# Performance work log

Measured on AMD Instinct MI355X. Metric: run time of the kernel, lower is better.

## Reference

```python
import jax, jax.numpy as jnp
import numpy as np

NUM_NODES = 8192
IN_FEATURES = 1024
OUT_FEATURES = 512
NUM_EDGES = 262144  # avg degree 32


def setup_inputs() -> dict:
    key = jax.random.key(0)
    k_x, k_w, k_b, k_src, k_dst = jax.random.split(key, 5)
    x = jax.random.normal(k_x, (NUM_NODES, IN_FEATURES), dtype=jnp.float32)
    # torch nn.Linear layout: weight [out, in], bias [out]
    W = jax.random.normal(k_w, (OUT_FEATURES, IN_FEATURES), dtype=jnp.float32) * (1.0 / np.sqrt(IN_FEATURES))
    b = jax.random.normal(k_b, (OUT_FEATURES,), dtype=jnp.float32) * 0.01
    src = jax.random.randint(k_src, (NUM_EDGES,), 0, NUM_NODES, dtype=jnp.int64)
    dst = jax.random.randint(k_dst, (NUM_EDGES,), 0, NUM_NODES, dtype=jnp.int64)
    edge_index = jnp.stack([src, dst], axis=0)
    return {"x": x, "W": W, "b": b, "edge_index": edge_index, "num_nodes": NUM_NODES}


def reference(x, W, b, edge_index, num_nodes):
    # Faithful to the torch module: build dense adjacency from edge list
    # (duplicate edges collapse to 1.0 via assignment semantics),
    # linear, (dropout p=0 -> identity), dense adj @ hidden, relu.
    adj = jnp.zeros((num_nodes, num_nodes), dtype=x.dtype)
    adj = adj.at[edge_index[0], edge_index[1]].set(1.0)
    hidden = x @ W.T + b            # [N, out]
    support = adj @ hidden          # [N, out] aggregation over neighbors
    return jax.nn.relu(support)
```

## Files before the change

kernel.cpp:

```cpp
#include <hip/hip_runtime.h>

#define N_NODES 8192
#define IN_F    1024
#define OUT_F   512
#define N_EDGES 262144
#define STRIDE  96
#define NBLK    64
#define EPB     (N_EDGES / NBLK)

#define HID_OFF     0u
#define WB_OFF      8388608u
#define DEG_OFF     9437184u
#define COL_OFF     9469952u
#define BH_OFF      12615680u
#define BO_OFF      14712832u
#define MAX_DEG     STRIDE

typedef short  bf16x8 __attribute__((ext_vector_type(8)));
typedef float  f32x4  __attribute__((ext_vector_type(4)));

__device__ __forceinline__ unsigned f2bf(float f) {
    unsigned u = __float_as_uint(f);
    u += 0x7fffu + ((u >> 16) & 1u);
    return u >> 16;
}

__device__ __forceinline__ float bflo(unsigned u) { return __uint_as_float(u << 16); }
__device__ __forceinline__ float bfhi(unsigned u) { return __uint_as_float(u & 0xffff0000u); }

__device__ __forceinline__ void ld_lds16(const void* g, void* l) {
    __builtin_amdgcn_global_load_lds(
        (const __attribute__((address_space(1))) void*)g,
        (__attribute__((address_space(3))) void*)l, 16, 0, 0);
}

#define NW8 (OUT_F * IN_F / 8)
__global__ __launch_bounds__(256) void prep_hist(const float* __restrict__ w,
                                                 unsigned short* __restrict__ wb,
                                                 const int* __restrict__ src,
                                                 int* __restrict__ blkhist) {
    __shared__ int h[N_NODES];
    const int bid = blockIdx.x;
    const int tid = threadIdx.x;

    if (bid < 256) {
        int i = bid * 256 + tid;
        const f32x4* p = (const f32x4*)w + (size_t)i * 2;
        f32x4 v0 = __builtin_nontemporal_load(p);
        f32x4 v1 = __builtin_nontemporal_load(p + 1);
        uint4 o;
        o.x = f2bf(v0.x) | (f2bf(v0.y) << 16);
        o.y = f2bf(v0.z) | (f2bf(v0.w) << 16);
        o.z = f2bf(v1.x) | (f2bf(v1.y) << 16);
        o.w = f2bf(v1.z) | (f2bf(v1.w) << 16);
        *((uint4*)wb + i) = o;
        return;
    }
    const int b = bid - 256;
    for (int i = tid; i < N_NODES; i += 256) h[i] = 0;
    __syncthreads();
    const int e0 = b * EPB;
#pragma unroll
    for (int j = 0; j < EPB / 256; ++j)
        atomicAdd(&h[src[e0 + j * 256 + tid]], 1);
    __syncthreads();
    for (int i = tid; i < N_NODES; i += 256)
        blkhist[b * N_NODES + i] = h[i];
}

__global__ __launch_bounds__(256) void scan_b(const int* __restrict__ blkhist,
                                              int* __restrict__ boff,
                                              int* __restrict__ deg) {
    const int i = blockIdx.x * 256 + threadIdx.x;
    int s = 0;
#pragma unroll 8
    for (int b = 0; b < NBLK; ++b) {
        int t = blkhist[b * N_NODES + i];
        boff[b * N_NODES + i] = s;
        s += t;
    }
    deg[i] = s;
}

__global__ __launch_bounds__(256, 4) void gemm_place(const float* __restrict__ X,
                                                     const unsigned short* __restrict__ Wb,
                                                     const float* __restrict__ bias,
                                                     unsigned short* __restrict__ H,
                                                     const int* __restrict__ src,
                                                     const int* __restrict__ dst,
                                                     const int* __restrict__ boff,
                                                     int* __restrict__ col) {
    __shared__ int smem[N_NODES];
    const int bid = blockIdx.x;
    const int tid = threadIdx.x;

    if (bid >= 1024) {
        const int b = bid - 1024;
        for (int i = tid; i < N_NODES; i += 256) smem[i] = 0;
        __syncthreads();
        const int e0 = b * EPB;
#pragma unroll
        for (int j = 0; j < EPB / 256; ++j) {
            int e = e0 + j * 256 + tid;
            int s = src[e];
            int r = boff[b * N_NODES + s] + atomicAdd(&smem[s], 1);
            if (r < STRIDE) col[s * STRIDE + r] = dst[e];
        }
        return;
    }

    unsigned short* As = (unsigned short*)smem;
    unsigned short* Bs = (unsigned short*)smem + 4096;
    const int lane = tid & 63;
    const int wave = tid >> 6;
    const int row0 = (bid & 127) * 64;
    const int col0 = (bid >> 7) * 64;
    const int wm   = (wave & 1) * 32;
    const int wn   = (wave >> 1) * 32;
    const int fm   = lane & 15;
    const int fm7  = fm & 7;
    const int q    = lane >> 4;

    f32x4 acc[2][2];
#pragma unroll
    for (int i = 0; i < 2; ++i)
#pragma unroll
        for (int j = 0; j < 2; ++j) acc[i][j] = (f32x4)0.f;

    const int ar   = tid >> 2;
    const int ak4  = tid & 3;
    const int ar7  = ar & 7;
    unsigned short* As_w0 = As + ar * 64 + ((ak4 * 2)     ^ ar7) * 8;
    unsigned short* As_w1 = As + ar * 64 + ((ak4 * 2 + 1) ^ ar7) * 8;
    const float* xrow = &X[(size_t)(row0 + ar) * IN_F + ak4 * 16];

    const int br = tid >> 3;
    const int bk = ((tid & 7) ^ (br & 7)) * 8;

    for (int k0 = 0; k0 < IN_F; k0 += 64) {
        const f32x4* px = (const f32x4*)(xrow + k0);
        f32x4 v0 = px[0], v1 = px[1], v2 = px[2], v3 = px[3];
        ld_lds16(Wb + (size_t)(col0 + br) * IN_F + k0 + bk,      Bs + tid * 8);
        ld_lds16(Wb + (size_t)(col0 + br + 32) * IN_F + k0 + bk, Bs + (tid + 256) * 8);
        uint4 pa, pb;
        pa.x = f2bf(v0.x) | (f2bf(v0.y) << 16);
        pa.y = f2bf(v0.z) | (f2bf(v0.w) << 16);
        pa.z = f2bf(v1.x) | (f2bf(v1.y) << 16);
        pa.w = f2bf(v1.z) | (f2bf(v1.w) << 16);
        pb.x = f2bf(v2.x) | (f2bf(v2.y) << 16);
        pb.y = f2bf(v2.z) | (f2bf(v2.w) << 16);
        pb.z = f2bf(v3.x) | (f2bf(v3.y) << 16);
        pb.w = f2bf(v3.z) | (f2bf(v3.w) << 16);
        *(uint4*)As_w0 = pa;
        *(uint4*)As_w1 = pb;
        __syncthreads();

#pragma unroll
        for (int s = 0; s < 2; ++s) {
            const int kq = s * 4 + q;
            bf16x8 a[2], b[2];
#pragma unroll
            for (int mi = 0; mi < 2; ++mi)
                a[mi] = *(const bf16x8*)&As[(((wm + mi * 16 + fm) << 3) + (kq ^ fm7)) << 3];
#pragma unroll
            for (int ni = 0; ni < 2; ++ni)
                b[ni] = *(const bf16x8*)&Bs[(((wn + ni * 16 + fm) << 3) + (kq ^ fm7)) << 3];
#pragma unroll
            for (int mi = 0; mi < 2; ++mi)
#pragma unroll
                for (int ni = 0; ni < 2; ++ni)
                    acc[mi][ni] = __builtin_amdgcn_mfma_f32_16x16x32_bf16(
                        a[mi], b[ni], acc[mi][ni], 0, 0, 0);
        }
        __syncthreads();
    }

    const int cm = (lane >> 4) * 4;
#pragma unroll
    for (int ni = 0; ni < 2; ++ni) {
        const int c = col0 + wn + ni * 16 + fm;
        const float bv = bias[c];
#pragma unroll
        for (int mi = 0; mi < 2; ++mi) {
#pragma unroll
            for (int r = 0; r < 4; ++r) {
                const int row = row0 + wm + mi * 16 + cm + r;
                H[(size_t)row * OUT_F + c] = (unsigned short)f2bf(acc[mi][ni][r] + bv);
            }
        }
    }
}

__global__ __launch_bounds__(256) void aggregate(const unsigned short* __restrict__ H,
                                                 const int* __restrict__ dg,
                                                 const int* __restrict__ col,
                                                 float* __restrict__ out) {
    __shared__ int nbr[4][MAX_DEG];
    __shared__ int uniq[4][MAX_DEG];
    __shared__ int wcnt[4];
    const int wave = threadIdx.x >> 6;
    const int lane = threadIdx.x & 63;
    const int v    = blockIdx.x * 4 + wave;
    int d = dg[v];
    if (d > MAX_DEG) d = MAX_DEG;

    if (lane == 0) wcnt[wave] = 0;
    int id0 = -1, id1 = -1;
    if (lane < d)      { id0 = col[v * STRIDE + lane];      nbr[wave][lane]      = id0; }
    if (64 + lane < d) { id1 = col[v * STRIDE + 64 + lane]; nbr[wave][64 + lane] = id1; }
    __builtin_amdgcn_wave_barrier();

    bool k0 = (lane < d);
    const int lim0 = k0 ? lane : 0;
    for (int j = 0; j < lim0; ++j) k0 = k0 & (nbr[wave][j] != id0);
    bool k1 = (64 + lane < d);
    const int lim1 = k1 ? (64 + lane) : 0;
    for (int j = 0; j < lim1; ++j) k1 = k1 & (nbr[wave][j] != id1);
    if (k0) uniq[wave][atomicAdd(&wcnt[wave], 1)] = id0;
    if (k1) uniq[wave][atomicAdd(&wcnt[wave], 1)] = id1;
    __builtin_amdgcn_wave_barrier();
    const int n  = wcnt[wave];
    const int f0 = lane * 8;

    float a0=0,a1=0,a2=0,a3=0,a4=0,a5=0,a6=0,a7=0;
    int e = 0;
    for (; e + 4 <= n; e += 4) {
        const int i0 = uniq[wave][e], i1 = uniq[wave][e+1],
                  i2 = uniq[wave][e+2], i3 = uniq[wave][e+3];
        uint4 h0 = *(const uint4*)&H[(size_t)i0 * OUT_F + f0];
        uint4 h1 = *(const uint4*)&H[(size_t)i1 * OUT_F + f0];
        uint4 h2 = *(const uint4*)&H[(size_t)i2 * OUT_F + f0];
        uint4 h3 = *(const uint4*)&H[(size_t)i3 * OUT_F + f0];
        a0 += bflo(h0.x)+bflo(h1.x)+bflo(h2.x)+bflo(h3.x);
        a1 += bfhi(h0.x)+bfhi(h1.x)+bfhi(h2.x)+bfhi(h3.x);
        a2 += bflo(h0.y)+bflo(h1.y)+bflo(h2.y)+bflo(h3.y);
        a3 += bfhi(h0.y)+bfhi(h1.y)+bfhi(h2.y)+bfhi(h3.y);
        a4 += bflo(h0.z)+bflo(h1.z)+bflo(h2.z)+bflo(h3.z);
        a5 += bfhi(h0.z)+bfhi(h1.z)+bfhi(h2.z)+bfhi(h3.z);
        a6 += bflo(h0.w)+bflo(h1.w)+bflo(h2.w)+bflo(h3.w);
        a7 += bfhi(h0.w)+bfhi(h1.w)+bfhi(h2.w)+bfhi(h3.w);
    }
    for (; e < n; ++e) {
        uint4 h0 = *(const uint4*)&H[(size_t)uniq[wave][e] * OUT_F + f0];
        a0 += bflo(h0.x); a1 += bfhi(h0.x);
        a2 += bflo(h0.y); a3 += bfhi(h0.y);
        a4 += bflo(h0.z); a5 += bfhi(h0.z);
        a6 += bflo(h0.w); a7 += bfhi(h0.w);
    }
    f32x4 o0 = {fmaxf(a0,0.f), fmaxf(a1,0.f), fmaxf(a2,0.f), fmaxf(a3,0.f)};
    f32x4 o1 = {fmaxf(a4,0.f), fmaxf(a5,0.f), fmaxf(a6,0.f), fmaxf(a7,0.f)};
    __builtin_nontemporal_store(o0, (f32x4*)&out[(size_t)v * OUT_F + f0]);
    __builtin_nontemporal_store(o1, (f32x4*)&out[(size_t)v * OUT_F + f0 + 4]);
}

extern "C" void kernel_launch(void* const* d_in, const int* in_sizes, int n_in,
                              void* d_out, int out_size, void* d_ws, size_t ws_size,
                              hipStream_t stream) {
    const float* x  = (const float*)d_in[0];
    const float* W  = (const float*)d_in[1];
    const float* b  = (const float*)d_in[2];
    const int*   ei = (const int*)d_in[3];
    float* out = (float*)d_out;

    char* ws = (char*)d_ws;
    unsigned short* H       = (unsigned short*)(ws + HID_OFF);
    unsigned short* Wb      = (unsigned short*)(ws + WB_OFF);
    int*            deg     = (int*)(ws + DEG_OFF);
    int*            col     = (int*)(ws + COL_OFF);
    int*            blkhist = (int*)(ws + BH_OFF);
    int*            boff    = (int*)(ws + BO_OFF);

    const int* src = ei;
    const int* dst = ei + N_EDGES;

    prep_hist<<<256 + NBLK, 256, 0, stream>>>(W, Wb, src, blkhist);
    scan_b<<<N_NODES / 256, 256, 0, stream>>>(blkhist, boff, deg);
    gemm_place<<<1024 + NBLK, 256, 0, stream>>>(x, Wb, b, H, src, dst, boff, col);
    aggregate<<<N_NODES / 4, 256, 0, stream>>>(H, deg, col, out);
}
```

Before: 153.1 us.

## Double-buffer GEMM LDS tiles and convert fp32 W to bf16 in-kernel

Drops the separate W-to-bf16 pre-pass and instead loads fp32 W tiles directly in the GEMM, converting them with packed bf16 conversion intrinsics. The GEMM main loop becomes double-buffered: the next tile's global loads are issued before the current tile's MFMAs, and there is one barrier per iteration instead of two. This removes the Wb workspace and shrinks the first kernel to a histogram only. In exchange, W is read as fp32 by every block (twice the bytes of bf16 per reload), and the kernel uses more LDS and more registers at 4 blocks per CU.

Measured after the change: 151.1 us. About the same (-1.4%).

```diff
diff --git a/kernel.cpp b/kernel.cpp
--- a/kernel.cpp
+++ b/kernel.cpp
@@ -1,4 +1,5 @@
 #include <hip/hip_runtime.h>
+#include <hip/hip_bf16.h>
 
 #define N_NODES 8192
 #define IN_F    1024
@@ -9,15 +10,16 @@
 #define EPB     (N_EDGES / NBLK)
 
 #define HID_OFF     0u
-#define WB_OFF      8388608u
-#define DEG_OFF     9437184u
-#define COL_OFF     9469952u
-#define BH_OFF      12615680u
-#define BO_OFF      14712832u
+#define DEG_OFF     8388608u
+#define COL_OFF     8421376u
+#define BH_OFF      11567104u
+#define BO_OFF      13664256u
 #define MAX_DEG     STRIDE
 
 typedef short  bf16x8 __attribute__((ext_vector_type(8)));
 typedef float  f32x4  __attribute__((ext_vector_type(4)));
+
+#define PIPE_BARRIER() __asm__ __volatile__("s_waitcnt lgkmcnt(0)\ns_barrier" ::: "memory")
 
 __device__ __forceinline__ unsigned f2bf(float f) {
     unsigned u = __float_as_uint(f);
@@ -28,35 +30,21 @@
 __device__ __forceinline__ float bflo(unsigned u) { return __uint_as_float(u << 16); }
 __device__ __forceinline__ float bfhi(unsigned u) { return __uint_as_float(u & 0xffff0000u); }
 
-__device__ __forceinline__ void ld_lds16(const void* g, void* l) {
-    __builtin_amdgcn_global_load_lds(
-        (const __attribute__((address_space(1))) void*)g,
-        (__attribute__((address_space(3))) void*)l, 16, 0, 0);
-}
-
-#define NW8 (OUT_F * IN_F / 8)
-__global__ __launch_bounds__(256) void prep_hist(const float* __restrict__ w,
-                                                 unsigned short* __restrict__ wb,
-                                                 const int* __restrict__ src,
-                                                 int* __restrict__ blkhist) {
+__device__ __forceinline__ uint2 pkcvt(f32x4 v) {
+    float2 p0 = {v.x, v.y}, p1 = {v.z, v.w};
+    __hip_bfloat162 b0 = __float22bfloat162_rn(p0);
+    __hip_bfloat162 b1 = __float22bfloat162_rn(p1);
+    uint2 r;
+    r.x = *(const unsigned*)&b0;
+    r.y = *(const unsigned*)&b1;
+    return r;
+}
+
+__global__ __launch_bounds__(256) void hist(const int* __restrict__ src,
+                                            int* __restrict__ blkhist) {
     __shared__ int h[N_NODES];
-    const int bid = blockIdx.x;
+    const int b   = blockIdx.x;
     const int tid = threadIdx.x;
-
-    if (bid < 256) {
-        int i = bid * 256 + tid;
-        const f32x4* p = (const f32x4*)w + (size_t)i * 2;
-        f32x4 v0 = __builtin_nontemporal_load(p);
-        f32x4 v1 = __builtin_nontemporal_load(p + 1);
-        uint4 o;
-        o.x = f2bf(v0.x) | (f2bf(v0.y) << 16);
-        o.y = f2bf(v0.z) | (f2bf(v0.w) << 16);
-        o.z = f2bf(v1.x) | (f2bf(v1.y) << 16);
-        o.w = f2bf(v1.z) | (f2bf(v1.w) << 16);
-        *((uint4*)wb + i) = o;
-        return;
-    }
-    const int b = bid - 256;
     for (int i = tid; i < N_NODES; i += 256) h[i] = 0;
     __syncthreads();
     const int e0 = b * EPB;
@@ -83,7 +71,7 @@
 }
 
 __global__ __launch_bounds__(256, 4) void gemm_place(const float* __restrict__ X,
-                                                     const unsigned short* __restrict__ Wb,
+                                                     const float* __restrict__ W,
                                                      const float* __restrict__ bias,
                                                      unsigned short* __restrict__ H,
                                                      const int* __restrict__ src,
@@ -109,8 +97,9 @@
         return;
     }
 
-    unsigned short* As = (unsigned short*)smem;
-    unsigned short* Bs = (unsigned short*)smem + 4096;
+    unsigned short* As[2] = {(unsigned short*)smem,        (unsigned short*)smem + 8192};
+    unsigned short* Bs[2] = {(unsigned short*)smem + 4096, (unsigned short*)smem + 12288};
+
     const int lane = tid & 63;
     const int wave = tid >> 6;
     const int row0 = (bid & 127) * 64;
@@ -127,52 +116,64 @@
 #pragma unroll
         for (int j = 0; j < 2; ++j) acc[i][j] = (f32x4)0.f;
 
-    const int ar   = tid >> 2;
-    const int ak4  = tid & 3;
-    const int ar7  = ar & 7;
-    unsigned short* As_w0 = As + ar * 64 + ((ak4 * 2)     ^ ar7) * 8;
-    unsigned short* As_w1 = As + ar * 64 + ((ak4 * 2 + 1) ^ ar7) * 8;
-    const float* xrow = &X[(size_t)(row0 + ar) * IN_F + ak4 * 16];
-
-    const int br = tid >> 3;
-    const int bk = ((tid & 7) ^ (br & 7)) * 8;
-
-    for (int k0 = 0; k0 < IN_F; k0 += 64) {
-        const f32x4* px = (const f32x4*)(xrow + k0);
-        f32x4 v0 = px[0], v1 = px[1], v2 = px[2], v3 = px[3];
-        ld_lds16(Wb + (size_t)(col0 + br) * IN_F + k0 + bk,      Bs + tid * 8);
-        ld_lds16(Wb + (size_t)(col0 + br + 32) * IN_F + k0 + bk, Bs + (tid + 256) * 8);
-        uint4 pa, pb;
-        pa.x = f2bf(v0.x) | (f2bf(v0.y) << 16);
-        pa.y = f2bf(v0.z) | (f2bf(v0.w) << 16);
-        pa.z = f2bf(v1.x) | (f2bf(v1.y) << 16);
-        pa.w = f2bf(v1.z) | (f2bf(v1.w) << 16);
-        pb.x = f2bf(v2.x) | (f2bf(v2.y) << 16);
-        pb.y = f2bf(v2.z) | (f2bf(v2.w) << 16);
-        pb.z = f2bf(v3.x) | (f2bf(v3.y) << 16);
-        pb.w = f2bf(v3.z) | (f2bf(v3.w) << 16);
-        *(uint4*)As_w0 = pa;
-        *(uint4*)As_w1 = pb;
-        __syncthreads();
-
+    const int u  = tid & 15;
+    const int rr = tid >> 4;
+    const float* gA = X + (size_t)(row0 + rr) * IN_F + 4 * u;
+    const float* gB = W + (size_t)(col0 + rr) * IN_F + 4 * u;
+    int lws[4];
+#pragma unroll
+    for (int j = 0; j < 4; ++j)
+        lws[j] = (rr + 16 * j) * 64 + (((u >> 1) ^ (rr & 7)) * 8) + (u & 1) * 4;
+
+    f32x4 va[4], vb[4];
+#pragma unroll
+    for (int j = 0; j < 4; ++j) {
+        va[j] = *(const f32x4*)(gA + (size_t)j * 16 * IN_F);
+        vb[j] = *(const f32x4*)(gB + (size_t)j * 16 * IN_F);
+    }
+#pragma unroll
+    for (int j = 0; j < 4; ++j) {
+        *(uint2*)(As[0] + lws[j]) = pkcvt(va[j]);
+        *(uint2*)(Bs[0] + lws[j]) = pkcvt(vb[j]);
+    }
+    PIPE_BARRIER();
+
+#pragma unroll
+    for (int k = 0; k < IN_F / 64; ++k) {
+        const int cur = k & 1;
+        if (k + 1 < IN_F / 64) {
+            const float* pa = gA + (size_t)(k + 1) * 64;
+            const float* pb = gB + (size_t)(k + 1) * 64;
+#pragma unroll
+            for (int j = 0; j < 4; ++j) {
+                va[j] = *(const f32x4*)(pa + (size_t)j * 16 * IN_F);
+                vb[j] = *(const f32x4*)(pb + (size_t)j * 16 * IN_F);
+            }
+        }
+        unsigned short* Ac = As[cur];
+        unsigned short* Bc = Bs[cur];
 #pragma unroll
         for (int s = 0; s < 2; ++s) {
             const int kq = s * 4 + q;
-            bf16x8 a[2], b[2];
-#pragma unroll
-            for (int mi = 0; mi < 2; ++mi)
-                a[mi] = *(const bf16x8*)&As[(((wm + mi * 16 + fm) << 3) + (kq ^ fm7)) << 3];
-#pragma unroll
-            for (int ni = 0; ni < 2; ++ni)
-                b[ni] = *(const bf16x8*)&Bs[(((wn + ni * 16 + fm) << 3) + (kq ^ fm7)) << 3];
-#pragma unroll
-            for (int mi = 0; mi < 2; ++mi)
-#pragma unroll
-                for (int ni = 0; ni < 2; ++ni)
-                    acc[mi][ni] = __builtin_amdgcn_mfma_f32_16x16x32_bf16(
-                        a[mi], b[ni], acc[mi][ni], 0, 0, 0);
-        }
-        __syncthreads();
+            bf16x8 a0 = *(const bf16x8*)&Ac[(((wm      + fm) << 3) + (kq ^ fm7)) << 3];
+            bf16x8 a1 = *(const bf16x8*)&Ac[(((wm + 16 + fm) << 3) + (kq ^ fm7)) << 3];
+            bf16x8 b0 = *(const bf16x8*)&Bc[(((wn      + fm) << 3) + (kq ^ fm7)) << 3];
+            bf16x8 b1 = *(const bf16x8*)&Bc[(((wn + 16 + fm) << 3) + (kq ^ fm7)) << 3];
+            acc[0][0] = __builtin_amdgcn_mfma_f32_16x16x32_bf16(a0, b0, acc[0][0], 0, 0, 0);
+            acc[0][1] = __builtin_amdgcn_mfma_f32_16x16x32_bf16(a0, b1, acc[0][1], 0, 0, 0);
+            acc[1][0] = __builtin_amdgcn_mfma_f32_16x16x32_bf16(a1, b0, acc[1][0], 0, 0, 0);
+            acc[1][1] = __builtin_amdgcn_mfma_f32_16x16x32_bf16(a1, b1, acc[1][1], 0, 0, 0);
+        }
+        if (k + 1 < IN_F / 64) {
+            unsigned short* An = As[1 - cur];
+            unsigned short* Bn = Bs[1 - cur];
+#pragma unroll
+            for (int j = 0; j < 4; ++j) {
+                *(uint2*)(An + lws[j]) = pkcvt(va[j]);
+                *(uint2*)(Bn + lws[j]) = pkcvt(vb[j]);
+            }
+            PIPE_BARRIER();
+        }
     }
 
     const int cm = (lane >> 4) * 4;
@@ -264,7 +265,6 @@
 
     char* ws = (char*)d_ws;
     unsigned short* H       = (unsigned short*)(ws + HID_OFF);
-    unsigned short* Wb      = (unsigned short*)(ws + WB_OFF);
     int*            deg     = (int*)(ws + DEG_OFF);
     int*            col     = (int*)(ws + COL_OFF);
     int*            blkhist = (int*)(ws + BH_OFF);
@@ -273,8 +273,8 @@
     const int* src = ei;
     const int* dst = ei + N_EDGES;
 
-    prep_hist<<<256 + NBLK, 256, 0, stream>>>(W, Wb, src, blkhist);
+    hist<<<NBLK, 256, 0, stream>>>(src, blkhist);
     scan_b<<<N_NODES / 256, 256, 0, stream>>>(blkhist, boff, deg);
-    gemm_place<<<1024 + NBLK, 256, 0, stream>>>(x, Wb, b, H, src, dst, boff, col);
+    gemm_place<<<1024 + NBLK, 256, 0, stream>>>(x, W, b, H, src, dst, boff, col);
     aggregate<<<N_NODES / 4, 256, 0, stream>>>(H, deg, col, out);
 }
```
